# Kernel tuning notes

Measured on AMD Instinct MI355X. Metric: run time of the kernel, lower is better.

The kernel has to match this reference:

```python
import jax, jax.numpy as jnp
import numpy as np

N, D = 128, 512  # batch, hypercube dim (in_features == n_2d_layers == out_features)

def setup_inputs() -> dict:
    key = jax.random.key(0)
    k1, k2, k3 = jax.random.split(key, 3)
    bound = 1.0 / np.sqrt(D)
    x = jax.random.normal(k1, (N, D, D), dtype=jnp.float32)
    # kaiming_uniform_(a=sqrt(5)) on (in, layers, out) ~ U(-1/sqrt(fan_in), 1/sqrt(fan_in)) scale
    w = jax.random.uniform(k2, (D, D, D), dtype=jnp.float32, minval=-bound, maxval=bound)
    b = jax.random.uniform(k3, (D, D), dtype=jnp.float32, minval=-bound, maxval=bound)
    return {"x": x, "w": w, "b": b}

def reference(x, w, b):
    # Original: (x.expand((L, *x.shape)).movedim(0,-2) * w).sum(-1) + b
    # which reduces to out[n,i,j] = sum_k x[n,i,k] * w[i,j,k] + b[i,j]
    # (w axes: (in_features, n_2d_layers, out_features), all equal D)
    return jnp.einsum('nik,ijk->nij', x, w) + b
```

## Files before the change

kernel.cpp:

```cpp
#include <hip/hip_runtime.h>


#define Nn 128
#define Dd 512
#define CHUNK 16
#define NCHUNK (Dd / CHUNK)

typedef __attribute__((ext_vector_type(8))) short bf16x8;
typedef __attribute__((ext_vector_type(4))) short bf16x4;
typedef __attribute__((ext_vector_type(4))) float f32x4;

__device__ __forceinline__ short f2bf(float f) {
    unsigned u = __builtin_bit_cast(unsigned, f);
    u += 0x7FFFu + ((u >> 16) & 1u);
    return (short)(u >> 16);
}

__global__ __launch_bounds__(512, 4)
void linear3d_kernel(const float* __restrict__ x,
                     const float* __restrict__ w,
                     const float* __restrict__ b,
                     float* __restrict__ out) {
    const int i    = blockIdx.x;
    const int tid  = threadIdx.x;
    const int lane = tid & 63;
    const int wid  = tid >> 6;

    __shared__ short lds[2 * CHUNK * Dd];

    const float* xi = x + (size_t)i * Dd;
    const float* wi = w + (size_t)i * Dd * Dd;

    float4 wreg[4];
    #pragma unroll
    for (int p = 0; p < 4; ++p)
        wreg[p] = *(const float4*)(wi + (size_t)(tid + p * 512) * 4);

    bf16x8 xf[16];
    #pragma unroll 4
    for (int r = 0; r < 4; ++r) {
        __syncthreads();
        #pragma unroll
        for (int p = 0; p < 8; ++p) {
            int idx4 = tid + p * 512;
            int row  = idx4 >> 7;
            int c4   = idx4 & 127;
            float4 v = *(const float4*)(xi + (size_t)(r * 32 + row) * (Dd * Dd) + c4 * 4);
            bf16x4 h = { f2bf(v.x), f2bf(v.y), f2bf(v.z), f2bf(v.w) };
            int byte = row * 1024 + c4 * 8;
            byte ^= (row & 7) << 4;
            *(bf16x4*)((char*)lds + byte) = h;
        }
        __syncthreads();
        if ((wid >> 1) == r) {
            int row = (wid & 1) * 16 + (lane & 15);
            #pragma unroll
            for (int s = 0; s < 16; ++s) {
                int byte = row * 1024 + s * 64 + (lane >> 4) * 16;
                byte ^= (row & 7) << 4;
                xf[s] = *(const bf16x8*)((const char*)lds + byte);
            }
        }
    }
    __syncthreads();

    #pragma unroll
    for (int p = 0; p < 4; ++p) {
        int idx4 = tid + p * 512;
        int row  = idx4 >> 7;
        int c4   = idx4 & 127;
        bf16x4 h = { f2bf(wreg[p].x), f2bf(wreg[p].y), f2bf(wreg[p].z), f2bf(wreg[p].w) };
        int byte = row * 1024 + c4 * 8;
        byte ^= (row & 7) << 4;
        *(bf16x4*)((char*)lds + byte) = h;
    }
    __syncthreads();

    const int nb = wid * 16;
    float* outbase = out + (size_t)i * Dd;

    for (int c = 0; c < NCHUNK; ++c) {
        if (c + 1 < NCHUNK) {
            const float* src = wi + (size_t)(c + 1) * (CHUNK * Dd);
            #pragma unroll
            for (int p = 0; p < 4; ++p)
                wreg[p] = *(const float4*)(src + (size_t)(tid + p * 512) * 4);
        }

        const char* buf = (const char*)lds + (c & 1) * (CHUNK * Dd * 2);
        f32x4 acc = {0.f, 0.f, 0.f, 0.f};
        #pragma unroll
        for (int s = 0; s < 16; ++s) {
            int row  = lane & 15;
            int byte = row * 1024 + s * 64 + (lane >> 4) * 16;
            byte ^= (row & 7) << 4;
            bf16x8 wf = *(const bf16x8*)(buf + byte);
            acc = __builtin_amdgcn_mfma_f32_16x16x32_bf16(xf[s], wf, acc, 0, 0, 0);
        }

        float bias = b[i * Dd + c * CHUNK + (lane & 15)];
        #pragma unroll
        for (int r = 0; r < 4; ++r) {
            int n = nb + (lane >> 4) * 4 + r;
            outbase[(size_t)n * (Dd * Dd) + c * CHUNK + (lane & 15)] = acc[r] + bias;
        }

        __syncthreads();
        if (c + 1 < NCHUNK) {
            char* dst = (char*)lds + ((c + 1) & 1) * (CHUNK * Dd * 2);
            #pragma unroll
            for (int p = 0; p < 4; ++p) {
                int idx4 = tid + p * 512;
                int row  = idx4 >> 7;
                int c4   = idx4 & 127;
                bf16x4 h = { f2bf(wreg[p].x), f2bf(wreg[p].y), f2bf(wreg[p].z), f2bf(wreg[p].w) };
                int byte = row * 1024 + c4 * 8;
                byte ^= (row & 7) << 4;
                *(bf16x4*)(dst + byte) = h;
            }
        }
        __syncthreads();
    }
}

extern "C" void kernel_launch(void* const* d_in, const int* in_sizes, int n_in,
                              void* d_out, int out_size, void* d_ws, size_t ws_size,
                              hipStream_t stream) {
    const float* x = (const float*)d_in[0];
    const float* w = (const float*)d_in[1];
    const float* b = (const float*)d_in[2];
    float* out = (float*)d_out;
    linear3d_kernel<<<dim3(Dd), dim3(512), 0, stream>>>(x, w, b, out);
}
```

Before: 201.8 us.

## Prefetch weight chunks two ahead and use one barrier per chunk

```diff
diff --git a/kernel.cpp b/kernel.cpp
--- a/kernel.cpp
+++ b/kernel.cpp
@@ -31,10 +31,13 @@
     const float* xi = x + (size_t)i * Dd;
     const float* wi = w + (size_t)i * Dd * Dd;
 
-    float4 wreg[4];
+    float4 wA[4], wB[4];
     #pragma unroll
     for (int p = 0; p < 4; ++p)
-        wreg[p] = *(const float4*)(wi + (size_t)(tid + p * 512) * 4);
+        wA[p] = *(const float4*)(wi + (size_t)(tid + p * 512) * 4);
+    #pragma unroll
+    for (int p = 0; p < 4; ++p)
+        wB[p] = *(const float4*)(wi + (size_t)(CHUNK * Dd) + (size_t)(tid + p * 512) * 4);
 
     bf16x8 xf[16];
     #pragma unroll 4
@@ -69,7 +72,7 @@
         int idx4 = tid + p * 512;
         int row  = idx4 >> 7;
         int c4   = idx4 & 127;
-        bf16x4 h = { f2bf(wreg[p].x), f2bf(wreg[p].y), f2bf(wreg[p].z), f2bf(wreg[p].w) };
+        bf16x4 h = { f2bf(wA[p].x), f2bf(wA[p].y), f2bf(wA[p].z), f2bf(wA[p].w) };
         int byte = row * 1024 + c4 * 8;
         byte ^= (row & 7) << 4;
         *(bf16x4*)((char*)lds + byte) = h;
@@ -78,49 +81,58 @@
 
     const int nb = wid * 16;
     float* outbase = out + (size_t)i * Dd;
+    float bias_cur = b[i * Dd + (lane & 15)];
 
-    for (int c = 0; c < NCHUNK; ++c) {
-        if (c + 1 < NCHUNK) {
-            const float* src = wi + (size_t)(c + 1) * (CHUNK * Dd);
-            #pragma unroll
-            for (int p = 0; p < 4; ++p)
-                wreg[p] = *(const float4*)(src + (size_t)(tid + p * 512) * 4);
-        }
+#define ITER(c, WISS, WCONV)  do {                                             \
+    if ((c) + 2 < NCHUNK) {                                                    \
+        const float* src = wi + (size_t)((c) + 2) * (CHUNK * Dd);              \
+        _Pragma("unroll")                                                      \
+        for (int p = 0; p < 4; ++p)                                            \
+            WISS[p] = *(const float4*)(src + (size_t)(tid + p * 512) * 4);     \
+    }                                                                          \
+    float bias_next = bias_cur;                                                \
+    if ((c) + 1 < NCHUNK) bias_next = b[i * Dd + ((c) + 1) * CHUNK + (lane & 15)]; \
+    {                                                                          \
+        const char* buf = (const char*)lds + (((c) & 1) * (CHUNK * Dd * 2));   \
+        f32x4 acc = {0.f, 0.f, 0.f, 0.f};                                      \
+        _Pragma("unroll")                                                      \
+        for (int s = 0; s < 16; ++s) {                                         \
+            int row  = lane & 15;                                              \
+            int byte = row * 1024 + s * 64 + (lane >> 4) * 16;                 \
+            byte ^= (row & 7) << 4;                                            \
+            bf16x8 wf = *(const bf16x8*)(buf + byte);                          \
+            acc = __builtin_amdgcn_mfma_f32_16x16x32_bf16(xf[s], wf, acc, 0, 0, 0); \
+        }                                                                      \
+        _Pragma("unroll")                                                      \
+        for (int r = 0; r < 4; ++r) {                                          \
+            int n = nb + (lane >> 4) * 4 + r;                                  \
+            outbase[(size_t)n * (Dd * Dd) + (c) * CHUNK + (lane & 15)] = acc[r] + bias_cur; \
+        }                                                                      \
+    }                                                                          \
+    if ((c) + 1 < NCHUNK) {                                                    \
+        char* dst = (char*)lds + ((((c) + 1) & 1) * (CHUNK * Dd * 2));         \
+        _Pragma("unroll")                                                      \
+        for (int p = 0; p < 4; ++p) {                                          \
+            int idx4 = tid + p * 512;                                          \
+            int row  = idx4 >> 7;                                              \
+            int c4   = idx4 & 127;                                             \
+            bf16x4 h = { f2bf(WCONV[p].x), f2bf(WCONV[p].y), f2bf(WCONV[p].z), f2bf(WCONV[p].w) }; \
+            int byte = row * 1024 + c4 * 8;                                    \
+            byte ^= (row & 7) << 4;                                            \
+            *(bf16x4*)(dst + byte) = h;                                        \
+        }                                                                      \
+    }                                                                          \
+    bias_cur = bias_next;                                                      \
+    asm volatile("s_waitcnt lgkmcnt(0)" ::: "memory");                         \
+    __builtin_amdgcn_s_barrier();                                              \
+    asm volatile("" ::: "memory");                                             \
+} while (0)
 
-        const char* buf = (const char*)lds + (c & 1) * (CHUNK * Dd * 2);
-        f32x4 acc = {0.f, 0.f, 0.f, 0.f};
-        #pragma unroll
-        for (int s = 0; s < 16; ++s) {
-            int row  = lane & 15;
-            int byte = row * 1024 + s * 64 + (lane >> 4) * 16;
-            byte ^= (row & 7) << 4;
-            bf16x8 wf = *(const bf16x8*)(buf + byte);
-            acc = __builtin_amdgcn_mfma_f32_16x16x32_bf16(xf[s], wf, acc, 0, 0, 0);
-        }
-
-        float bias = b[i * Dd + c * CHUNK + (lane & 15)];
-        #pragma unroll
-        for (int r = 0; r < 4; ++r) {
-            int n = nb + (lane >> 4) * 4 + r;
-            outbase[(size_t)n * (Dd * Dd) + c * CHUNK + (lane & 15)] = acc[r] + bias;
-        }
-
-        __syncthreads();
-        if (c + 1 < NCHUNK) {
-            char* dst = (char*)lds + ((c + 1) & 1) * (CHUNK * Dd * 2);
-            #pragma unroll
-            for (int p = 0; p < 4; ++p) {
-                int idx4 = tid + p * 512;
-                int row  = idx4 >> 7;
-                int c4   = idx4 & 127;
-                bf16x4 h = { f2bf(wreg[p].x), f2bf(wreg[p].y), f2bf(wreg[p].z), f2bf(wreg[p].w) };
-                int byte = row * 1024 + c4 * 8;
-                byte ^= (row & 7) << 4;
-                *(bf16x4*)(dst + byte) = h;
-            }
-        }
-        __syncthreads();
+    for (int c = 0; c < NCHUNK; c += 2) {
+        ITER(c,     wA, wB);
+        ITER(c + 1, wB, wA);
     }
+#undef ITER
 }
 
 extern "C" void kernel_launch(void* const* d_in, const int* in_sizes, int n_in,
```

After: 267.3 us. +32.5%, slower.

## Stream weight chunks via global_load_lds into fp32 LDS staging buffer

Applied to the files above, without the earlier changes.

```diff
diff --git a/kernel.cpp b/kernel.cpp
--- a/kernel.cpp
+++ b/kernel.cpp
@@ -1,10 +1,9 @@
 #include <hip/hip_runtime.h>
 
 
-#define Nn 128
 #define Dd 512
 #define CHUNK 16
-#define NCHUNK (Dd / CHUNK)
+#define NCHUNK 32
 
 typedef __attribute__((ext_vector_type(8))) short bf16x8;
 typedef __attribute__((ext_vector_type(4))) short bf16x4;
@@ -14,6 +13,12 @@
     unsigned u = __builtin_bit_cast(unsigned, f);
     u += 0x7FFFu + ((u >> 16) & 1u);
     return (short)(u >> 16);
+}
+
+__device__ __forceinline__ void glds16(const float* g, float* l) {
+    __builtin_amdgcn_global_load_lds(
+        (const __attribute__((address_space(1))) void*)g,
+        (__attribute__((address_space(3))) void*)l, 16, 0, 0);
 }
 
 __global__ __launch_bounds__(512, 4)
@@ -26,16 +31,21 @@
     const int lane = tid & 63;
     const int wid  = tid >> 6;
 
-    __shared__ short lds[2 * CHUNK * Dd];
+    __shared__ float f32s[CHUNK * Dd];
+    __shared__ short b16[2][CHUNK * Dd];
+    __shared__ float ldsb[Dd];
 
     const float* xi = x + (size_t)i * Dd;
     const float* wi = w + (size_t)i * Dd * Dd;
 
-    float4 wreg[4];
+    ldsb[tid] = b[i * Dd + tid];
+
     #pragma unroll
-    for (int p = 0; p < 4; ++p)
-        wreg[p] = *(const float4*)(wi + (size_t)(tid + p * 512) * 4);
+    for (int q = 0; q < 4; ++q)
+        glds16(wi + (size_t)(wid * 256 + q * 64 + lane) * 4,
+               &f32s[(wid * 256 + q * 64) * 4]);
 
+    short* xstage = &b16[0][0];
     bf16x8 xf[16];
     #pragma unroll 4
     for (int r = 0; r < 4; ++r) {
@@ -43,13 +53,12 @@
         #pragma unroll
         for (int p = 0; p < 8; ++p) {
             int idx4 = tid + p * 512;
-            int row  = idx4 >> 7;
-            int c4   = idx4 & 127;
+            int row  = idx4 >> 7, c4 = idx4 & 127;
             float4 v = *(const float4*)(xi + (size_t)(r * 32 + row) * (Dd * Dd) + c4 * 4);
             bf16x4 h = { f2bf(v.x), f2bf(v.y), f2bf(v.z), f2bf(v.w) };
             int byte = row * 1024 + c4 * 8;
             byte ^= (row & 7) << 4;
-            *(bf16x4*)((char*)lds + byte) = h;
+            *(bf16x4*)((char*)xstage + byte) = h;
         }
         __syncthreads();
         if ((wid >> 1) == r) {
@@ -58,7 +67,7 @@
             for (int s = 0; s < 16; ++s) {
                 int byte = row * 1024 + s * 64 + (lane >> 4) * 16;
                 byte ^= (row & 7) << 4;
-                xf[s] = *(const bf16x8*)((const char*)lds + byte);
+                xf[s] = *(const bf16x8*)((const char*)xstage + byte);
             }
         }
     }
@@ -67,59 +76,68 @@
     #pragma unroll
     for (int p = 0; p < 4; ++p) {
         int idx4 = tid + p * 512;
-        int row  = idx4 >> 7;
-        int c4   = idx4 & 127;
-        bf16x4 h = { f2bf(wreg[p].x), f2bf(wreg[p].y), f2bf(wreg[p].z), f2bf(wreg[p].w) };
-        int byte = row * 1024 + c4 * 8;
+        int row = idx4 >> 7, cu = idx4 & 127;
+        float4 v = *(const float4*)(f32s + idx4 * 4);
+        bf16x4 h = { f2bf(v.x), f2bf(v.y), f2bf(v.z), f2bf(v.w) };
+        int byte = row * 1024 + cu * 8;
         byte ^= (row & 7) << 4;
-        *(bf16x4*)((char*)lds + byte) = h;
+        *(bf16x4*)((char*)&b16[0][0] + byte) = h;
     }
-    __syncthreads();
+    asm volatile("s_waitcnt lgkmcnt(0)" ::: "memory");
+    __builtin_amdgcn_s_barrier();
 
+    #pragma unroll
+    for (int q = 0; q < 4; ++q)
+        glds16(wi + (size_t)(CHUNK * Dd) + (size_t)(wid * 256 + q * 64 + lane) * 4,
+               &f32s[(wid * 256 + q * 64) * 4]);
+
+    const int row16 = lane & 15;
     const int nb = wid * 16;
     float* outbase = out + (size_t)i * Dd;
 
     for (int c = 0; c < NCHUNK; ++c) {
-        if (c + 1 < NCHUNK) {
-            const float* src = wi + (size_t)(c + 1) * (CHUNK * Dd);
-            #pragma unroll
-            for (int p = 0; p < 4; ++p)
-                wreg[p] = *(const float4*)(src + (size_t)(tid + p * 512) * 4);
-        }
-
-        const char* buf = (const char*)lds + (c & 1) * (CHUNK * Dd * 2);
+        const char* buf = (const char*)&b16[c & 1][0];
         f32x4 acc = {0.f, 0.f, 0.f, 0.f};
         #pragma unroll
         for (int s = 0; s < 16; ++s) {
-            int row  = lane & 15;
-            int byte = row * 1024 + s * 64 + (lane >> 4) * 16;
-            byte ^= (row & 7) << 4;
+            int byte = row16 * 1024 + s * 64 + (lane >> 4) * 16;
+            byte ^= (row16 & 7) << 4;
             bf16x8 wf = *(const bf16x8*)(buf + byte);
             acc = __builtin_amdgcn_mfma_f32_16x16x32_bf16(xf[s], wf, acc, 0, 0, 0);
         }
-
-        float bias = b[i * Dd + c * CHUNK + (lane & 15)];
+        float bias = ldsb[c * 16 + row16];
         #pragma unroll
         for (int r = 0; r < 4; ++r) {
             int n = nb + (lane >> 4) * 4 + r;
-            outbase[(size_t)n * (Dd * Dd) + c * CHUNK + (lane & 15)] = acc[r] + bias;
+            outbase[(size_t)n * (Dd * Dd) + c * CHUNK + row16] = acc[r] + bias;
         }
 
-        __syncthreads();
         if (c + 1 < NCHUNK) {
-            char* dst = (char*)lds + ((c + 1) & 1) * (CHUNK * Dd * 2);
+            asm volatile("s_waitcnt lgkmcnt(0) vmcnt(4)" ::: "memory");
+            __builtin_amdgcn_s_barrier();
+
+            char* dstb = (char*)&b16[(c + 1) & 1][0];
             #pragma unroll
             for (int p = 0; p < 4; ++p) {
                 int idx4 = tid + p * 512;
-                int row  = idx4 >> 7;
-                int c4   = idx4 & 127;
-                bf16x4 h = { f2bf(wreg[p].x), f2bf(wreg[p].y), f2bf(wreg[p].z), f2bf(wreg[p].w) };
-                int byte = row * 1024 + c4 * 8;
+                int row = idx4 >> 7, cu = idx4 & 127;
+                float4 v = *(const float4*)(f32s + idx4 * 4);
+                bf16x4 h = { f2bf(v.x), f2bf(v.y), f2bf(v.z), f2bf(v.w) };
+                int byte = row * 1024 + cu * 8;
                 byte ^= (row & 7) << 4;
-                *(bf16x4*)(dst + byte) = h;
+                *(bf16x4*)(dstb + byte) = h;
+            }
+            asm volatile("s_waitcnt lgkmcnt(0)" ::: "memory");
+            __builtin_amdgcn_s_barrier();
+
+            if (c + 2 < NCHUNK) {
+                const float* src = wi + (size_t)(c + 2) * (CHUNK * Dd);
+                #pragma unroll
+                for (int q = 0; q < 4; ++q)
+                    glds16(src + (size_t)(wid * 256 + q * 64 + lane) * 4,
+                           &f32s[(wid * 256 + q * 64) * 4]);
             }
         }
-        __syncthreads();
     }
 }
 
```

Result: faster. 184.8 us (-8.4%).

## Stream weights via global_load_lds with a 4-stage half-chunk pipeline

Applied to the files above, without the earlier changes.

```diff
diff --git a/kernel.cpp b/kernel.cpp
--- a/kernel.cpp
+++ b/kernel.cpp
@@ -1,10 +1,9 @@
 #include <hip/hip_runtime.h>
 
 
-#define Nn 128
 #define Dd 512
-#define CHUNK 16
-#define NCHUNK (Dd / CHUNK)
+#define DD (512 * 512)
+#define NPH 64
 
 typedef __attribute__((ext_vector_type(8))) short bf16x8;
 typedef __attribute__((ext_vector_type(4))) short bf16x4;
@@ -14,6 +13,12 @@
     unsigned u = __builtin_bit_cast(unsigned, f);
     u += 0x7FFFu + ((u >> 16) & 1u);
     return (short)(u >> 16);
+}
+
+__device__ __forceinline__ void glds16(const float* g, float* l) {
+    __builtin_amdgcn_global_load_lds(
+        (const __attribute__((address_space(1))) void*)g,
+        (__attribute__((address_space(3))) void*)l, 16, 0, 0);
 }
 
 __global__ __launch_bounds__(512, 4)
@@ -26,101 +31,142 @@
     const int lane = tid & 63;
     const int wid  = tid >> 6;
 
-    __shared__ short lds[2 * CHUNK * Dd];
+    __shared__ float f32h[4][4096];
+    __shared__ short b16h[2][4096];
 
     const float* xi = x + (size_t)i * Dd;
-    const float* wi = w + (size_t)i * Dd * Dd;
+    const float* wi = w + (size_t)i * DD;
+    const int row16 = lane & 15;
+    const int cg16  = (lane >> 4) * 16;
 
-    float4 wreg[4];
     #pragma unroll
-    for (int p = 0; p < 4; ++p)
-        wreg[p] = *(const float4*)(wi + (size_t)(tid + p * 512) * 4);
+    for (int h0 = 0; h0 < 3; ++h0) {
+        const float* src = wi + (size_t)(h0 >> 1) * (16 * Dd) + (h0 & 1) * 256;
+        #pragma unroll
+        for (int q = 0; q < 2; ++q) {
+            int rl = wid * 2 + q;
+            glds16(src + (size_t)rl * Dd + lane * 4, &f32h[h0][rl * 256]);
+        }
+    }
 
+    short* xs = &b16h[0][0];
     bf16x8 xf[16];
-    #pragma unroll 4
-    for (int r = 0; r < 4; ++r) {
+    for (int r = 0; r < 8; ++r) {
         __syncthreads();
         #pragma unroll
-        for (int p = 0; p < 8; ++p) {
+        for (int p = 0; p < 4; ++p) {
             int idx4 = tid + p * 512;
-            int row  = idx4 >> 7;
-            int c4   = idx4 & 127;
-            float4 v = *(const float4*)(xi + (size_t)(r * 32 + row) * (Dd * Dd) + c4 * 4);
-            bf16x4 h = { f2bf(v.x), f2bf(v.y), f2bf(v.z), f2bf(v.w) };
-            int byte = row * 1024 + c4 * 8;
-            byte ^= (row & 7) << 4;
-            *(bf16x4*)((char*)lds + byte) = h;
+            int row = idx4 >> 7, c4 = idx4 & 127;
+            float4 v = *(const float4*)(xi + (size_t)(r * 16 + row) * DD + c4 * 4);
+            bf16x4 hh = { f2bf(v.x), f2bf(v.y), f2bf(v.z), f2bf(v.w) };
+            int byte = (row * 1024 + c4 * 8) ^ ((row & 7) << 4);
+            *(bf16x4*)((char*)xs + byte) = hh;
         }
         __syncthreads();
-        if ((wid >> 1) == r) {
-            int row = (wid & 1) * 16 + (lane & 15);
+        if (wid == r) {
             #pragma unroll
             for (int s = 0; s < 16; ++s) {
-                int byte = row * 1024 + s * 64 + (lane >> 4) * 16;
-                byte ^= (row & 7) << 4;
-                xf[s] = *(const bf16x8*)((const char*)lds + byte);
+                int byte = (row16 * 1024 + s * 64 + cg16) ^ ((row16 & 7) << 4);
+                xf[s] = *(const bf16x8*)((const char*)xs + byte);
             }
         }
     }
     __syncthreads();
 
-    #pragma unroll
-    for (int p = 0; p < 4; ++p) {
-        int idx4 = tid + p * 512;
-        int row  = idx4 >> 7;
-        int c4   = idx4 & 127;
-        bf16x4 h = { f2bf(wreg[p].x), f2bf(wreg[p].y), f2bf(wreg[p].z), f2bf(wreg[p].w) };
-        int byte = row * 1024 + c4 * 8;
-        byte ^= (row & 7) << 4;
-        *(bf16x4*)((char*)lds + byte) = h;
-    }
+#define CONVERT(FS, BS) do {                                                   \
+    _Pragma("unroll")                                                          \
+    for (int p = 0; p < 2; ++p) {                                              \
+        float4 v = *(const float4*)(&f32h[FS][p * 2048 + tid * 4]);            \
+        int rw = p * 8 + wid;                                                  \
+        bf16x4 hh = { f2bf(v.x), f2bf(v.y), f2bf(v.z), f2bf(v.w) };            \
+        int byte = (rw * 512 + lane * 8) ^ ((rw & 7) << 4);                    \
+        *(bf16x4*)((char*)&b16h[BS][0] + byte) = hh;                           \
+    }                                                                          \
+} while (0)
+
+#define GLDS_ISSUE(Hn, FB) do {                                                \
+    const float* src_ = wi + (size_t)((Hn) >> 1) * (16 * Dd) + ((Hn) & 1) * 256; \
+    _Pragma("unroll")                                                          \
+    for (int q = 0; q < 2; ++q) {                                              \
+        int rl = wid * 2 + q;                                                  \
+        glds16(src_ + (size_t)rl * Dd + lane * 4, &f32h[FB][rl * 256]);        \
+    }                                                                          \
+} while (0)
+
+#define COMPUTE(U, ACC) do {                                                   \
+    _Pragma("unroll")                                                          \
+    for (int s = 0; s < 8; ++s) {                                              \
+        int byte = (row16 * 512 + s * 64 + cg16) ^ ((row16 & 7) << 4);         \
+        bf16x8 wf = *(const bf16x8*)((const char*)&b16h[(U) & 1][0] + byte);   \
+        ACC = __builtin_amdgcn_mfma_f32_16x16x32_bf16(                         \
+            xf[((U) & 1) * 8 + s], wf, ACC, 0, 0, 0);                          \
+    }                                                                          \
+} while (0)
+
+#define ENDPH(VM) do {                                                         \
+    asm volatile("s_waitcnt vmcnt(" #VM ") lgkmcnt(0)" ::: "memory");          \
+    __builtin_amdgcn_s_barrier();                                              \
+} while (0)
+
+#define PH(H, U, ACC, VM) do {                                                 \
+    int h_ = (H);                                                              \
+    if (h_ + 3 < NPH) GLDS_ISSUE(h_ + 3, ((U) + 3) & 3);                       \
+    COMPUTE(U, ACC);                                                           \
+    CONVERT(((U) + 1) & 3, ((U) + 1) & 1);                                     \
+    ENDPH(VM);                                                                 \
+} while (0)
+
+#define PH3(H, VM) do {                                                        \
+    int h_ = (H);                                                              \
+    int j0 = (h_ - 3) * 8 + row16;                                             \
+    float bias0 = b[i * Dd + j0];                                              \
+    float bias1 = b[i * Dd + j0 + 16];                                         \
+    if (h_ + 3 < NPH) GLDS_ISSUE(h_ + 3, 2);                                   \
+    COMPUTE(3, acc1);                                                          \
+    if (h_ + 1 < NPH) CONVERT(0, 0);                                           \
+    _Pragma("unroll")                                                          \
+    for (int r_ = 0; r_ < 4; ++r_) {                                           \
+        int n_ = wid * 16 + (lane >> 4) * 4 + r_;                              \
+        float* op_ = out + (size_t)i * Dd + (size_t)n_ * DD;                   \
+        op_[j0]      = acc0[r_] + bias0;                                       \
+        op_[j0 + 16] = acc1[r_] + bias1;                                       \
+    }                                                                          \
+    ENDPH(VM);                                                                 \
+} while (0)
+
+    CONVERT(0, 0);
     __syncthreads();
 
-    const int nb = wid * 16;
-    float* outbase = out + (size_t)i * Dd;
+    f32x4 acc0 = {0.f, 0.f, 0.f, 0.f}, acc1 = {0.f, 0.f, 0.f, 0.f};
 
-    for (int c = 0; c < NCHUNK; ++c) {
-        if (c + 1 < NCHUNK) {
-            const float* src = wi + (size_t)(c + 1) * (CHUNK * Dd);
-            #pragma unroll
-            for (int p = 0; p < 4; ++p)
-                wreg[p] = *(const float4*)(src + (size_t)(tid + p * 512) * 4);
-        }
+    PH (0, 0, acc0, 2);
+    PH (1, 1, acc0, 2);
+    PH (2, 2, acc1, 2);
+    PH3(3, 12);
 
-        const char* buf = (const char*)lds + (c & 1) * (CHUNK * Dd * 2);
-        f32x4 acc = {0.f, 0.f, 0.f, 0.f};
-        #pragma unroll
-        for (int s = 0; s < 16; ++s) {
-            int row  = lane & 15;
-            int byte = row * 1024 + s * 64 + (lane >> 4) * 16;
-            byte ^= (row & 7) << 4;
-            bf16x8 wf = *(const bf16x8*)(buf + byte);
-            acc = __builtin_amdgcn_mfma_f32_16x16x32_bf16(xf[s], wf, acc, 0, 0, 0);
-        }
+    for (int t = 1; t < 15; ++t) {
+        int h = t * 4;
+        acc0 = (f32x4){0.f, 0.f, 0.f, 0.f};
+        PH (h,     0, acc0, 10);
+        PH (h + 1, 1, acc0, 2);
+        acc1 = (f32x4){0.f, 0.f, 0.f, 0.f};
+        PH (h + 2, 2, acc1, 2);
+        PH3(h + 3, 12);
+    }
 
-        float bias = b[i * Dd + c * CHUNK + (lane & 15)];
-        #pragma unroll
-        for (int r = 0; r < 4; ++r) {
-            int n = nb + (lane >> 4) * 4 + r;
-            outbase[(size_t)n * (Dd * Dd) + c * CHUNK + (lane & 15)] = acc[r] + bias;
-        }
+    acc0 = (f32x4){0.f, 0.f, 0.f, 0.f};
+    PH (60, 0, acc0, 10);
+    PH (61, 1, acc0, 0);
+    acc1 = (f32x4){0.f, 0.f, 0.f, 0.f};
+    PH (62, 2, acc1, 0);
+    PH3(63, 0);
 
-        __syncthreads();
-        if (c + 1 < NCHUNK) {
-            char* dst = (char*)lds + ((c + 1) & 1) * (CHUNK * Dd * 2);
-            #pragma unroll
-            for (int p = 0; p < 4; ++p) {
-                int idx4 = tid + p * 512;
-                int row  = idx4 >> 7;
-                int c4   = idx4 & 127;
-                bf16x4 h = { f2bf(wreg[p].x), f2bf(wreg[p].y), f2bf(wreg[p].z), f2bf(wreg[p].w) };
-                int byte = row * 1024 + c4 * 8;
-                byte ^= (row & 7) << 4;
-                *(bf16x4*)(dst + byte) = h;
-            }
-        }
-        __syncthreads();
-    }
+#undef PH3
+#undef PH
+#undef ENDPH
+#undef COMPUTE
+#undef GLDS_ISSUE
+#undef CONVERT
 }
 
 extern "C" void kernel_launch(void* const* d_in, const int* in_sizes, int n_in,
```

After: 206.3 us. 2.3% more time.
